# Performance work log

Measured on AMD Instinct MI355X. Metric: run time of the kernel, lower is better.

## Reference

```python
import jax, jax.numpy as jnp
import numpy as np

NUM_NODES = 100000
EMB_DIM = 64
OUT_C = 64
K = 3
NUM_EDGES = 1600000


def setup_inputs() -> dict:
    key = jax.random.key(0)
    k1, k2, k3, k4 = jax.random.split(key, 4)
    x_indices = jnp.arange(NUM_NODES, dtype=jnp.int64)
    ei = jax.random.randint(k1, (2, NUM_EDGES), 0, NUM_NODES, dtype=jnp.int64)
    # learned params: embedding table + final linear of SGConv
    emb_weight = jax.random.normal(k2, (NUM_NODES, EMB_DIM), dtype=jnp.float32)
    lin_w = jax.random.normal(k3, (OUT_C, EMB_DIM), dtype=jnp.float32) / np.sqrt(EMB_DIM)
    lin_b = jax.random.normal(k4, (OUT_C,), dtype=jnp.float32) * 0.01
    return {"x_indices": x_indices, "ei": ei, "emb_weight": emb_weight,
            "lin_w": lin_w, "lin_b": lin_b}


def _sgconv(x, ei, lin_w, lin_b, k_hops):
    """PyG SGConv: (D^-1/2 (A+I) D^-1/2)^K X, then Linear."""
    n = x.shape[0]
    row, col = ei[0], ei[1]
    loops = jnp.arange(n, dtype=ei.dtype)
    row = jnp.concatenate([row, loops])
    col = jnp.concatenate([col, loops])
    ones = jnp.ones(row.shape[0], dtype=x.dtype)
    deg = jax.ops.segment_sum(ones, col, num_segments=n)  # in-degree incl. self-loops
    dinv = jnp.where(deg > 0, jax.lax.rsqrt(deg), 0.0)
    norm = dinv[row] * dinv[col]  # [E+N]
    for _ in range(k_hops):
        # gather source features, scale, scatter-add to targets
        x = jax.ops.segment_sum(x[row] * norm[:, None], col, num_segments=n)
    return x @ lin_w.T + lin_b


def reference(x_indices, ei, emb_weight, lin_w, lin_b):
    x = emb_weight[x_indices]  # [N, EMB_DIM] embedding lookup
    return _sgconv(x, ei, lin_w, lin_b, K)
```

## Files before the change

kernel.cpp:

```cpp
#include <hip/hip_runtime.h>
#include <hip/hip_bf16.h>
#include <math.h>


#define FLAG_MX 0
#define FLAG_ME 1
#define SH 9
#define WC 512
#define CH 4096
#define RMASK 0x7FFFFFu

using short8 = __attribute__((ext_vector_type(8))) short;
using f32x4 = __attribute__((ext_vector_type(4))) float;

__device__ inline int idx_at(const void* p, long long i, int mode) {
    switch (mode) {
        case 1: return (int)((const long long*)p)[i];
        case 2: return (int)((const float*)p)[i];
        case 3: return (int)((const double*)p)[i];
        default: return ((const int*)p)[i];
    }
}

__device__ inline unsigned short f2bf(float f) {
    union { float f; unsigned u; } v; v.f = f;
    unsigned r = v.u + 0x7FFFu + ((v.u >> 16) & 1u);
    return (unsigned short)(r >> 16);
}
__device__ inline float bflo(unsigned d) { union { unsigned u; float f; } v; v.u = d << 16; return v.f; }
__device__ inline float bfhi(unsigned d) { union { unsigned u; float f; } v; v.u = d & 0xFFFF0000u; return v.f; }
__device__ inline unsigned pk(float a, float b) {
    return (unsigned)f2bf(a) | ((unsigned)f2bf(b) << 16);
}

__device__ int detect_me_block(const void* ei, int n, int* sbuf) {
    int t = threadIdx.x;
    int oke = 15;
    const int* w = (const int*)ei;
    const long long* L = (const long long*)ei;
    const float* f = (const float*)ei;
    const double* d = (const double*)ei;
    for (int k = t; k < 2048; k += 256) {
        if (!((unsigned)w[k] < (unsigned)n)) oke &= ~1;
        long long lv = L[k];
        if (!(lv >= 0 && lv < (long long)n)) oke &= ~2;
        float fv = f[k];
        if (!(fv >= 0.f && fv < (float)n && fv == truncf(fv))) oke &= ~4;
        double dv = d[k];
        if (!(dv >= 0.0 && dv < (double)n && dv == trunc(dv))) oke &= ~8;
    }
    sbuf[t] = oke;
    __syncthreads();
    for (int st = 128; st; st >>= 1) {
        if (t < st) sbuf[t] &= sbuf[t + st];
        __syncthreads();
    }
    int r = sbuf[0];
    __syncthreads();
    return (r & 2) ? 1 : (r & 8) ? 3 : (r & 4) ? 2 : 0;
}

__device__ int detect_mx_block(const void* xidx, int* sbuf) {
    int t = threadIdx.x;
    int okx = 15;
    const int* w = (const int*)xidx;
    const long long* L = (const long long*)xidx;
    const float* f = (const float*)xidx;
    const double* d = (const double*)xidx;
    for (int k = t; k < 2048; k += 256) {
        if (w[k] != k) okx &= ~1;
        if (L[k] != (long long)k) okx &= ~2;
        if (!(f[k] == (float)k)) okx &= ~4;
        if (!(d[k] == (double)k)) okx &= ~8;
    }
    sbuf[t] = okx;
    __syncthreads();
    for (int st = 128; st; st >>= 1) {
        if (t < st) sbuf[t] &= sbuf[t + st];
        __syncthreads();
    }
    int r = sbuf[0];
    __syncthreads();
    return (r & 2) ? 1 : (r & 8) ? 3 : (r & 4) ? 2 : 0;
}

__global__ void __launch_bounds__(256) k_p1(
        const void* __restrict__ ei, const void* __restrict__ xidx,
        long long E, int n, int NBUK, int NBLK,
        int* __restrict__ bhist, int* __restrict__ flags) {
    __shared__ int hist[256];
    __shared__ int sbuf[256];
    int t = threadIdx.x;
    int blk = blockIdx.x;
    int me = detect_me_block(ei, n, sbuf);
    if (blk == 0) {
        int mx = detect_mx_block(xidx, sbuf);
        if (t == 0) { flags[FLAG_ME] = me; flags[FLAG_MX] = mx; }
    }
    long long base = (long long)blk * CH;
    int cnt = (int)min((long long)CH, E - base);
    hist[t] = 0;
    __syncthreads();
    for (int i = t; i < cnt; i += 256) {
        int c = idx_at(ei, E + base + i, me);
        int b = min(c >> SH, NBUK - 1);
        atomicAdd(&hist[b], 1);
    }
    __syncthreads();
    if (t < NBUK) bhist[(size_t)t * NBLK + blk] = hist[t];
}

__global__ void __launch_bounds__(256) k_p2a(
        int* __restrict__ bhist, int* __restrict__ gcount, int NBLK) {
    __shared__ int s[256];
    int b = blockIdx.x;
    int t = threadIdx.x;
    int* row = bhist + (size_t)b * NBLK;
    int carry = 0;
    for (int base = 0; base < NBLK; base += 256) {
        int i = base + t;
        int v = (i < NBLK) ? row[i] : 0;
        s[t] = v;
        __syncthreads();
        for (int st = 1; st < 256; st <<= 1) {
            int add = (t >= st) ? s[t - st] : 0;
            __syncthreads();
            s[t] += add;
            __syncthreads();
        }
        if (i < NBLK) row[i] = carry + s[t] - v;
        int total = s[255];
        __syncthreads();
        carry += total;
    }
    if (t == 0) gcount[b] = carry;
}

__device__ void scan_gcount(const int* gcount, int NBUK, int* p, int* gb_ex) {
    int t = threadIdx.x;
    int v = (t < NBUK) ? gcount[t] : 0;
    p[t] = v;
    __syncthreads();
    for (int st = 1; st < 256; st <<= 1) {
        int add = (t >= st) ? p[t - st] : 0;
        __syncthreads();
        p[t] += add;
        __syncthreads();
    }
    gb_ex[t] = p[t] - v;
    __syncthreads();
}

__global__ void __launch_bounds__(256) k_p3(
        const void* __restrict__ ei, long long E, int n, int NBUK, int NBLK,
        const int* __restrict__ bhist, const int* __restrict__ gcount,
        unsigned* __restrict__ gstag, const int* __restrict__ flags) {
    __shared__ int hist[256], lbase[256], rsv[256], lcur[256], s[256], gb[256];
    __shared__ unsigned stage[CH];
    int t = threadIdx.x;
    int blk = blockIdx.x;
    scan_gcount(gcount, NBUK, s, gb);
    long long base = (long long)blk * CH;
    int cnt = (int)min((long long)CH, E - base);
    int me = flags[FLAG_ME];
    hist[t] = 0;
    __syncthreads();
    for (int i = t; i < cnt; i += 256) {
        int c = idx_at(ei, E + base + i, me);
        atomicAdd(&hist[min(c >> SH, NBUK - 1)], 1);
    }
    __syncthreads();
    int v = hist[t];
    s[t] = v;
    __syncthreads();
    for (int st = 1; st < 256; st <<= 1) {
        int add = (t >= st) ? s[t - st] : 0;
        __syncthreads();
        s[t] += add;
        __syncthreads();
    }
    lbase[t] = s[t] - v;
    lcur[t] = s[t] - v;
    if (t < NBUK) rsv[t] = gb[t] + bhist[(size_t)t * NBLK + blk];
    __syncthreads();
    for (int i = t; i < cnt; i += 256) {
        long long e = base + i;
        int r = idx_at(ei, e, me);
        int c = idx_at(ei, E + e, me);
        int b = min(c >> SH, NBUK - 1);
        unsigned pkv = ((unsigned)r & RMASK) |
                       (((unsigned)(c - (b << SH)) & (WC - 1)) << 23);
        int slot = atomicAdd(&lcur[b], 1);
        stage[slot] = pkv;
    }
    __syncthreads();
    for (int i = t; i < cnt; i += 256) {
        unsigned pkv = stage[i];
        int lo = 0, hi = NBUK - 1;
        while (lo < hi) {
            int mid = (lo + hi + 1) >> 1;
            if (lbase[mid] <= i) lo = mid; else hi = mid - 1;
        }
        gstag[rsv[lo] + (i - lbase[lo])] = pkv;
    }
}

__global__ void __launch_bounds__(256) k_p4(
        const unsigned* __restrict__ gstag, const int* __restrict__ gcount,
        int* __restrict__ off, float* __restrict__ dinv,
        int* __restrict__ rowidx, const void* __restrict__ xidx,
        const float4* __restrict__ emb4, uint4* __restrict__ zS,
        const int* __restrict__ flags, int n, int NBUK, long long E) {
    __shared__ int hist[WC], lofs[WC], cur[WC], p[256], gb[256];
    int t = threadIdx.x;
    int b = blockIdx.x;
    int cbase = b << SH;
    scan_gcount(gcount, NBUK, p, gb);
    int e0 = gb[b];
    int e1 = e0 + gcount[b];
    int cnt = e1 - e0;
    if (b == NBUK - 1 && t == 0) off[n] = e1;
    hist[t] = 0; hist[t + 256] = 0;
    __syncthreads();
    for (int i = t; i < cnt; i += 256) {
        int cl = (int)(gstag[e0 + i] >> 23);
        atomicAdd(&hist[cl], 1);
    }
    __syncthreads();
    int a0 = hist[2 * t], a1 = hist[2 * t + 1];
    int s2 = a0 + a1;
    p[t] = s2;
    __syncthreads();
    for (int st = 1; st < 256; st <<= 1) {
        int add = (t >= st) ? p[t - st] : 0;
        __syncthreads();
        p[t] += add;
        __syncthreads();
    }
    int excl = p[t] - s2;
    lofs[2 * t] = excl;       cur[2 * t] = excl;
    lofs[2 * t + 1] = excl + a0; cur[2 * t + 1] = excl + a0;
    __syncthreads();
    int ncols = n - cbase;
    if (ncols < 0) ncols = 0;
    if (ncols > WC) ncols = WC;
    for (int j = t; j < ncols; j += 256) {
        off[cbase + j] = e0 + lofs[j];
        dinv[cbase + j] = rsqrtf((float)(hist[j] + 1));
    }
    for (int i = t; i < cnt; i += 256) {
        unsigned pkv = gstag[e0 + i];
        int cl = (int)(pkv >> 23);
        int slot = atomicAdd(&cur[cl], 1);
        rowidx[e0 + slot] = (int)(pkv & RMASK);
    }
    int mx = flags[FLAG_MX];
    for (int i = t; i < ncols * 8; i += 256) {
        int j = i >> 3, q = i & 7;
        int node = cbase + j;
        int xi = idx_at(xidx, node, mx);
        if ((unsigned)xi >= (unsigned)n) xi = 0;
        float dv = rsqrtf((float)(hist[j] + 1));
        float4 a = emb4[(long long)xi * 16 + q * 2];
        float4 bb = emb4[(long long)xi * 16 + q * 2 + 1];
        uint4 o;
        o.x = pk(a.x * dv, a.y * dv);
        o.y = pk(a.z * dv, a.w * dv);
        o.z = pk(bb.x * dv, bb.y * dv);
        o.w = pk(bb.z * dv, bb.w * dv);
        zS[(long long)node * 8 + q] = o;
    }
}

__device__ inline void acc8(float* acc, uint4 s) {
    acc[0] += bflo(s.x); acc[1] += bfhi(s.x);
    acc[2] += bflo(s.y); acc[3] += bfhi(s.y);
    acc[4] += bflo(s.z); acc[5] += bfhi(s.z);
    acc[6] += bflo(s.w); acc[7] += bfhi(s.w);
}

__global__ void __launch_bounds__(256) k_hop(
        const uint4* __restrict__ zin, uint4* __restrict__ zout,
        const float* __restrict__ dinv, const int* __restrict__ off,
        const int* __restrict__ rowidx, int n, int last) {
    int tid = blockIdx.x * 256 + threadIdx.x;
    int node = tid >> 3;
    int q = tid & 7;
    if (node >= n) return;
    float acc[8];
    {
        uint4 s = zin[(long long)node * 8 + q];
        acc[0] = bflo(s.x); acc[1] = bfhi(s.x);
        acc[2] = bflo(s.y); acc[3] = bfhi(s.y);
        acc[4] = bflo(s.z); acc[5] = bfhi(s.z);
        acc[6] = bflo(s.w); acc[7] = bfhi(s.w);
    }
    int e0 = off[node], e1 = off[node + 1];
    int e = e0;
    for (; e + 4 <= e1; e += 4) {
        int r0 = rowidx[e + 0];
        int r1 = rowidx[e + 1];
        int r2 = rowidx[e + 2];
        int r3 = rowidx[e + 3];
        uint4 s0 = zin[(long long)r0 * 8 + q];
        uint4 s1 = zin[(long long)r1 * 8 + q];
        uint4 s2 = zin[(long long)r2 * 8 + q];
        uint4 s3 = zin[(long long)r3 * 8 + q];
        acc8(acc, s0);
        acc8(acc, s1);
        acc8(acc, s2);
        acc8(acc, s3);
    }
    for (; e < e1; e++) {
        int r = rowidx[e];
        acc8(acc, zin[(long long)r * 8 + q]);
    }
    float d = dinv[node];
    float sc = last ? d : d * d;
    uint4 o;
    o.x = pk(acc[0] * sc, acc[1] * sc);
    o.y = pk(acc[2] * sc, acc[3] * sc);
    o.z = pk(acc[4] * sc, acc[5] * sc);
    o.w = pk(acc[6] * sc, acc[7] * sc);
    zout[(long long)node * 8 + q] = o;
}

__global__ void __launch_bounds__(256) k_lin_mfma(
        const short8* __restrict__ x8, const float* __restrict__ w,
        const float* __restrict__ b, float* __restrict__ out, int n, int ntiles) {
    int lane = threadIdx.x & 63;
    int wv = threadIdx.x >> 6;
    int col = lane & 15, quad = lane >> 4;

    short8 bw[4][2];
#pragma unroll
    for (int tN = 0; tN < 4; tN++)
#pragma unroll
        for (int s = 0; s < 2; s++) {
            const float* src = w + (tN * 16 + col) * 64 + s * 32 + quad * 8;
            short8 v;
#pragma unroll
            for (int j = 0; j < 8; j++) v[j] = (short)f2bf(src[j]);
            bw[tN][s] = v;
        }
    float bv[4];
#pragma unroll
    for (int tN = 0; tN < 4; tN++) bv[tN] = b[tN * 16 + col];

    int tile = blockIdx.x * 4 + wv;
    if (tile >= ntiles) return;
    int node0 = tile * 16;

    short8 a[2];
    int m = node0 + col;
#pragma unroll
    for (int s = 0; s < 2; s++) {
        if (m < n) a[s] = x8[(size_t)m * 8 + s * 4 + quad];
        else a[s] = short8{0, 0, 0, 0, 0, 0, 0, 0};
    }
#pragma unroll
    for (int tN = 0; tN < 4; tN++) {
        f32x4 acc = {bv[tN], bv[tN], bv[tN], bv[tN]};
        acc = __builtin_amdgcn_mfma_f32_16x16x32_bf16(a[0], bw[tN][0], acc, 0, 0, 0);
        acc = __builtin_amdgcn_mfma_f32_16x16x32_bf16(a[1], bw[tN][1], acc, 0, 0, 0);
#pragma unroll
        for (int r = 0; r < 4; r++) {
            int node = node0 + quad * 4 + r;
            if (node < n) out[(size_t)node * 64 + tN * 16 + col] = acc[r];
        }
    }
}

extern "C" void kernel_launch(void* const* d_in, const int* in_sizes, int n_in,
                              void* d_out, int out_size, void* d_ws, size_t ws_size,
                              hipStream_t stream) {
    const void* xidx = d_in[0];
    const void* ei = d_in[1];
    const float* emb = (const float*)d_in[2];
    const float* w = (const float*)d_in[3];
    const float* b = (const float*)d_in[4];

    const int n = in_sizes[0];
    const long long E = in_sizes[1] / 2;
    int NBUK = (int)((n + WC - 1) >> SH);
    if (NBUK > 256) NBUK = 256;
    const int NBLK = (int)((E + CH - 1) / CH);

    char* p = (char*)d_ws;
    auto alloc = [&](size_t bytes) -> void* {
        void* r = (void*)p;
        p += (bytes + 255) & ~(size_t)255;
        return r;
    };
    int* flags = (int*)alloc(256);
    float* dinv = (float*)alloc((size_t)n * 4);
    int* off = (int*)alloc((size_t)(n + 1) * 4);
    int* gcount = (int*)alloc(257 * 4);
    int* bhist = (int*)alloc((size_t)NBLK * NBUK * 4);
    int* rowidx = (int*)alloc((size_t)E * 4);
    uint4* zA = (uint4*)alloc((size_t)n * 64 * 2);
    uint4* zS = (uint4*)d_out;

    unsigned* gstag;
    if ((size_t)E * 4 <= (size_t)n * 64 * 2)
        gstag = (unsigned*)((char*)d_out + (size_t)n * 64 * 2);
    else
        gstag = (unsigned*)alloc((size_t)E * 4);

    k_p1<<<NBLK, 256, 0, stream>>>(ei, xidx, E, n, NBUK, NBLK, bhist, flags);
    k_p2a<<<NBUK, 256, 0, stream>>>(bhist, gcount, NBLK);
    k_p3<<<NBLK, 256, 0, stream>>>(ei, E, n, NBUK, NBLK, bhist, gcount, gstag, flags);
    k_p4<<<NBUK, 256, 0, stream>>>(gstag, gcount, off, dinv, rowidx, xidx,
                                   (const float4*)emb, zS, flags, n, NBUK, E);

    const int gF = (n * 8 + 255) / 256;
    const int ntiles = (n + 15) / 16;
    const int gM = (ntiles + 3) / 4;

    k_hop<<<gF, 256, 0, stream>>>(zS, zA, dinv, off, rowidx, n, 0);
    k_hop<<<gF, 256, 0, stream>>>(zA, zS, dinv, off, rowidx, n, 0);
    k_hop<<<gF, 256, 0, stream>>>(zS, zA, dinv, off, rowidx, n, 1);
    k_lin_mfma<<<gM, 256, 0, stream>>>((const short8*)zA, w, b, (float*)d_out,
                                       n, ntiles);
}
```

Measured before the change: 282.7 us.

## Split embedding scaling out of CSR bucket kernel and widen buckets to 512 threads

Result: faster. 259.2 us (-8.3%).

```diff
diff --git a/kernel.cpp b/kernel.cpp
--- a/kernel.cpp
+++ b/kernel.cpp
@@ -151,6 +151,21 @@
     __syncthreads();
 }
 
+__device__ void scan_gcount_512(const int* gcount, int NBUK, int* p, int* gb_ex) {
+    int t = threadIdx.x;
+    int v = (t < 256) ? ((t < NBUK) ? gcount[t] : 0) : 0;
+    if (t < 256) p[t] = v;
+    __syncthreads();
+    for (int st = 1; st < 256; st <<= 1) {
+        int add = (t >= st && t < 256) ? p[t - st] : 0;
+        __syncthreads();
+        if (t < 256) p[t] += add;
+        __syncthreads();
+    }
+    if (t < 256) gb_ex[t] = p[t] - v;
+    __syncthreads();
+}
+
 __global__ void __launch_bounds__(256) k_p3(
         const void* __restrict__ ei, long long E, int n, int NBUK, int NBLK,
         const int* __restrict__ bhist, const int* __restrict__ gcount,
@@ -205,71 +220,71 @@
     }
 }
 
-__global__ void __launch_bounds__(256) k_p4(
+__global__ void __launch_bounds__(512) k_p4(
         const unsigned* __restrict__ gstag, const int* __restrict__ gcount,
         int* __restrict__ off, float* __restrict__ dinv,
-        int* __restrict__ rowidx, const void* __restrict__ xidx,
-        const float4* __restrict__ emb4, uint4* __restrict__ zS,
-        const int* __restrict__ flags, int n, int NBUK, long long E) {
-    __shared__ int hist[WC], lofs[WC], cur[WC], p[256], gb[256];
+        int* __restrict__ rowidx, int n, int NBUK) {
+    __shared__ int hist[WC], lofs[WC], cur[WC], p[512], gb[256];
     int t = threadIdx.x;
     int b = blockIdx.x;
     int cbase = b << SH;
-    scan_gcount(gcount, NBUK, p, gb);
+    scan_gcount_512(gcount, NBUK, p, gb);
     int e0 = gb[b];
     int e1 = e0 + gcount[b];
     int cnt = e1 - e0;
     if (b == NBUK - 1 && t == 0) off[n] = e1;
-    hist[t] = 0; hist[t + 256] = 0;
-    __syncthreads();
-    for (int i = t; i < cnt; i += 256) {
-        int cl = (int)(gstag[e0 + i] >> 23);
-        atomicAdd(&hist[cl], 1);
-    }
-    __syncthreads();
-    int a0 = hist[2 * t], a1 = hist[2 * t + 1];
-    int s2 = a0 + a1;
-    p[t] = s2;
-    __syncthreads();
-    for (int st = 1; st < 256; st <<= 1) {
+    hist[t] = 0;
+    __syncthreads();
+    for (int i = t; i < cnt; i += 512) {
+        atomicAdd(&hist[gstag[e0 + i] >> 23], 1);
+    }
+    __syncthreads();
+    int v = hist[t];
+    p[t] = v;
+    __syncthreads();
+    for (int st = 1; st < 512; st <<= 1) {
         int add = (t >= st) ? p[t - st] : 0;
         __syncthreads();
         p[t] += add;
         __syncthreads();
     }
-    int excl = p[t] - s2;
-    lofs[2 * t] = excl;       cur[2 * t] = excl;
-    lofs[2 * t + 1] = excl + a0; cur[2 * t + 1] = excl + a0;
+    int excl = p[t] - v;
+    lofs[t] = excl;
+    cur[t] = excl;
     __syncthreads();
     int ncols = n - cbase;
     if (ncols < 0) ncols = 0;
     if (ncols > WC) ncols = WC;
-    for (int j = t; j < ncols; j += 256) {
-        off[cbase + j] = e0 + lofs[j];
-        dinv[cbase + j] = rsqrtf((float)(hist[j] + 1));
-    }
-    for (int i = t; i < cnt; i += 256) {
+    if (t < ncols) {
+        off[cbase + t] = e0 + lofs[t];
+        dinv[cbase + t] = rsqrtf((float)(hist[t] + 1));
+    }
+    for (int i = t; i < cnt; i += 512) {
         unsigned pkv = gstag[e0 + i];
         int cl = (int)(pkv >> 23);
         int slot = atomicAdd(&cur[cl], 1);
         rowidx[e0 + slot] = (int)(pkv & RMASK);
     }
-    int mx = flags[FLAG_MX];
-    for (int i = t; i < ncols * 8; i += 256) {
-        int j = i >> 3, q = i & 7;
-        int node = cbase + j;
-        int xi = idx_at(xidx, node, mx);
-        if ((unsigned)xi >= (unsigned)n) xi = 0;
-        float dv = rsqrtf((float)(hist[j] + 1));
-        float4 a = emb4[(long long)xi * 16 + q * 2];
-        float4 bb = emb4[(long long)xi * 16 + q * 2 + 1];
-        uint4 o;
-        o.x = pk(a.x * dv, a.y * dv);
-        o.y = pk(a.z * dv, a.w * dv);
-        o.z = pk(bb.x * dv, bb.y * dv);
-        o.w = pk(bb.z * dv, bb.w * dv);
-        zS[(long long)node * 8 + q] = o;
-    }
+}
+
+__global__ void __launch_bounds__(256) k_z0(
+        const void* __restrict__ xidx, const float4* __restrict__ emb4,
+        const float* __restrict__ dinv, uint4* __restrict__ z, int n,
+        const int* __restrict__ flags) {
+    int i = blockIdx.x * 256 + threadIdx.x;
+    if (i >= n * 8) return;
+    int node = i >> 3, q = i & 7;
+    int xi = idx_at(xidx, node, flags[FLAG_MX]);
+    if ((unsigned)xi >= (unsigned)n) xi = 0;
+    float d = dinv[node];
+    float4 a = emb4[(long long)xi * 16 + q * 2];
+    float4 b = emb4[(long long)xi * 16 + q * 2 + 1];
+    uint4 o;
+    o.x = pk(a.x * d, a.y * d);
+    o.y = pk(a.z * d, a.w * d);
+    o.z = pk(b.x * d, b.y * d);
+    o.w = pk(b.z * d, b.w * d);
+    z[(long long)node * 8 + q] = o;
 }
 
 __device__ inline void acc8(float* acc, uint4 s) {
@@ -410,13 +425,13 @@
     k_p1<<<NBLK, 256, 0, stream>>>(ei, xidx, E, n, NBUK, NBLK, bhist, flags);
     k_p2a<<<NBUK, 256, 0, stream>>>(bhist, gcount, NBLK);
     k_p3<<<NBLK, 256, 0, stream>>>(ei, E, n, NBUK, NBLK, bhist, gcount, gstag, flags);
-    k_p4<<<NBUK, 256, 0, stream>>>(gstag, gcount, off, dinv, rowidx, xidx,
-                                   (const float4*)emb, zS, flags, n, NBUK, E);
+    k_p4<<<NBUK, 512, 0, stream>>>(gstag, gcount, off, dinv, rowidx, n, NBUK);
 
     const int gF = (n * 8 + 255) / 256;
     const int ntiles = (n + 15) / 16;
     const int gM = (ntiles + 3) / 4;
 
+    k_z0<<<gF, 256, 0, stream>>>(xidx, (const float4*)emb, dinv, zS, n, flags);
     k_hop<<<gF, 256, 0, stream>>>(zS, zA, dinv, off, rowidx, n, 0);
     k_hop<<<gF, 256, 0, stream>>>(zA, zS, dinv, off, rowidx, n, 0);
     k_hop<<<gF, 256, 0, stream>>>(zS, zA, dinv, off, rowidx, n, 1);
```
